# Kernel tuning notes

Measured on AMD Instinct MI355X. Metric: run time of the kernel, lower is better.

The kernel has to match this reference:

```python
import jax, jax.numpy as jnp
import numpy as np

N_NODES = 100_000
N_EDGES = 1_600_000
N_GRAPHS = 512
D_NODE = 128
H = 128
L_EXTRA = 2  # model_layer - 1


def _bn(x, g, b, eps=1e-5):
    # BatchNorm1d, training-mode math (biased batch variance), eval dropout = identity
    mu = jnp.mean(x, axis=0)
    var = jnp.var(x, axis=0)
    return g * (x - mu) * jax.lax.rsqrt(var + eps) + b


def _gin_conv(x, src, dst, W1, b1, bng, bnb, W2, b2):
    # GINConv (eps=0): mlp(x + sum_{j->i} x_j); mlp = Lin -> BN -> ReLU -> Lin
    agg = jax.ops.segment_sum(x[src], dst, num_segments=x.shape[0])
    h = x + agg
    h = jax.nn.relu(_bn(h @ W1 + b1, bng, bnb))
    return h @ W2 + b2


def setup_inputs():
    key = jax.random.key(0)
    ks = jax.random.split(key, 24)
    s = 0.05
    d = {}
    d["x"] = jax.random.normal(ks[0], (N_NODES, D_NODE), dtype=jnp.float32)
    d["edge_index"] = jax.random.randint(ks[1], (2, N_EDGES), 0, N_NODES, dtype=jnp.int32)
    d["batch"] = jnp.sort(jax.random.randint(ks[2], (N_NODES,), 0, N_GRAPHS, dtype=jnp.int32))
    d["vn_emb"] = jax.random.normal(ks[3], (1, H)) * s
    # conv1 MLP: Linear(D_NODE, 2H) -> BN -> ReLU -> Linear(2H, H)
    d["c1_W1"] = jax.random.normal(ks[4], (D_NODE, 2 * H)) * s
    d["c1_b1"] = jnp.zeros((2 * H,))
    d["c1_bng"] = jnp.ones((2 * H,))
    d["c1_bnb"] = jnp.zeros((2 * H,))
    d["c1_W2"] = jax.random.normal(ks[5], (2 * H, H)) * s
    d["c1_b2"] = jnp.zeros((H,))
    d["bn1_g"] = jnp.ones((H,))
    d["bn1_b"] = jnp.zeros((H,))
    # stacked extra GIN layers (model_layer - 1)
    d["cW1"] = jax.random.normal(ks[6], (L_EXTRA, H, 2 * H)) * s
    d["cb1"] = jnp.zeros((L_EXTRA, 2 * H))
    d["cbng"] = jnp.ones((L_EXTRA, 2 * H))
    d["cbnb"] = jnp.zeros((L_EXTRA, 2 * H))
    d["cW2"] = jax.random.normal(ks[7], (L_EXTRA, 2 * H, H)) * s
    d["cb2"] = jnp.zeros((L_EXTRA, H))
    d["bns_g"] = jnp.ones((L_EXTRA, H))
    d["bns_b"] = jnp.zeros((L_EXTRA, H))
    # virtual node MLP: Lin(H,2H)->BN->ReLU->Lin(2H,H)->BN->ReLU->Dropout
    d["vW1"] = jax.random.normal(ks[8], (H, 2 * H)) * s
    d["vb1"] = jnp.zeros((2 * H,))
    d["vbn1_g"] = jnp.ones((2 * H,))
    d["vbn1_b"] = jnp.zeros((2 * H,))
    d["vW2"] = jax.random.normal(ks[9], (2 * H, H)) * s
    d["vb2"] = jnp.zeros((H,))
    d["vbn2_g"] = jnp.ones((H,))
    d["vbn2_b"] = jnp.zeros((H,))
    return d


def reference(x, edge_index, batch, vn_emb, c1_W1, c1_b1, c1_bng, c1_bnb, c1_W2, c1_b2,
              bn1_g, bn1_b, cW1, cb1, cbng, cbnb, cW2, cb2, bns_g, bns_b,
              vW1, vb1, vbn1_g, vbn1_b, vW2, vb2, vbn2_g, vbn2_b):
    src, dst = edge_index[0], edge_index[1]
    # virtual node feature per graph: Embedding(1, H) indexed with zeros
    vfeat = jnp.broadcast_to(vn_emb[0], (N_GRAPHS, H))
    # layer 1: dropout is identity in eval mode
    post = jax.nn.relu(_bn(_gin_conv(x, src, dst, c1_W1, c1_b1, c1_bng, c1_bnb, c1_W2, c1_b2), bn1_g, bn1_b))
    for i in range(L_EXTRA):
        post = post + vfeat[batch]                       # virtual-node broadcast
        post = _bn(_gin_conv(post, src, dst, cW1[i], cb1[i], cbng[i], cbnb[i], cW2[i], cb2[i]), bns_g[i], bns_b[i])
        if i < L_EXTRA - 1:
            post = jax.nn.relu(post)
            pooled = jax.ops.segment_sum(post, batch, num_segments=N_GRAPHS)  # GlobalAddPool
            z = pooled + vfeat
            z = jax.nn.relu(_bn(z @ vW1 + vb1, vbn1_g, vbn1_b))
            vfeat = jax.nn.relu(_bn(z @ vW2 + vb2, vbn2_g, vbn2_b))
    # readout: global mean pool over nodes per graph
    counts = jax.ops.segment_sum(jnp.ones((x.shape[0],), post.dtype), batch, num_segments=N_GRAPHS)
    out = jax.ops.segment_sum(post, batch, num_segments=N_GRAPHS) / jnp.maximum(counts, 1.0)[:, None]
    return out
```

## Files before the change

kernel.cpp:

```cpp
#include <hip/hip_runtime.h>

#define NN 100000
#define NE 1600000
#define NG 512
#define DH 128
#define DH2 256
#define SCB 98
#define NSTRIPE 32

typedef __attribute__((ext_vector_type(8))) _Float16 h8;
typedef __attribute__((ext_vector_type(2))) _Float16 h2;
typedef __attribute__((ext_vector_type(4))) float f4;

static inline size_t align256(size_t x) { return (x + 255) & ~size_t(255); }

__global__ __launch_bounds__(256) void countslot_k(const int* __restrict__ ei,
                                                   int* __restrict__ cursor,
                                                   int* __restrict__ slot) {
    int i = blockIdx.x * blockDim.x + threadIdx.x;
    int e = i * 4;
    if (e >= NE) return;
    int4 d = *(const int4*)(ei + NE + e);
    int s0 = atomicAdd(&cursor[d.x], 1);
    int s1 = atomicAdd(&cursor[d.y], 1);
    int s2 = atomicAdd(&cursor[d.z], 1);
    int s3 = atomicAdd(&cursor[d.w], 1);
    int4 r; r.x = s0; r.y = s1; r.z = s2; r.w = s3;
    *(int4*)(slot + e) = r;
}

__global__ __launch_bounds__(256) void place_k(const int* __restrict__ ei,
                                               const int* __restrict__ rowptr,
                                               const int* __restrict__ slot,
                                               int* __restrict__ esrc) {
    int i = blockIdx.x * blockDim.x + threadIdx.x;
    int e = i * 4;
    if (e >= NE) return;
    int4 d = *(const int4*)(ei + NE + e);
    int4 sl = *(const int4*)(slot + e);
    int4 sr = *(const int4*)(ei + e);
    int r0 = rowptr[d.x];
    int r1 = rowptr[d.y];
    int r2 = rowptr[d.z];
    int r3 = rowptr[d.w];
    esrc[r0 + sl.x] = sr.x;
    esrc[r1 + sl.y] = sr.y;
    esrc[r2 + sl.z] = sr.z;
    esrc[r3 + sl.w] = sr.w;
}

__global__ __launch_bounds__(256) void scan1_k(const int* __restrict__ deg,
                                               int* __restrict__ part) {
    int i0 = blockIdx.x * 1024 + threadIdx.x * 4;
    int s = 0;
    if (i0 < NN) {
        int4 v = *(const int4*)(deg + i0);
        s = v.x + v.y + v.z + v.w;
    }
#pragma unroll
    for (int o = 1; o < 64; o <<= 1) s += __shfl_xor(s, o);
    __shared__ int ws[4];
    if ((threadIdx.x & 63) == 0) ws[threadIdx.x >> 6] = s;
    __syncthreads();
    if (threadIdx.x == 0) part[blockIdx.x] = ws[0] + ws[1] + ws[2] + ws[3];
}

__global__ void scan2_k(int* __restrict__ part, int* __restrict__ rowptr,
                        const int* __restrict__ batch, int* __restrict__ gcnt) {
    int t = threadIdx.x;
    __shared__ int wtot[2];
    int v = 0, s = 0;
    if (t < 128) {
        v = (t < SCB) ? part[t] : 0;
        s = v;
#pragma unroll
        for (int o = 1; o < 64; o <<= 1) {
            int u = __shfl_up(s, o);
            if ((t & 63) >= o) s += u;
        }
        if ((t & 63) == 63) wtot[t >> 6] = s;
    }
    __syncthreads();
    if (t < 128) {
        if (t >= 64) s += wtot[0];
        if (t < SCB) part[t] = s - v;
        if (t == SCB - 1) rowptr[NN] = s;
    }
    for (int g = t; g < NG; g += 256) {
        int lo = 0, hi = NN;
        while (lo < hi) { int m = (lo + hi) >> 1; if (batch[m] < g) lo = m + 1; else hi = m; }
        int b0 = lo;
        lo = 0; hi = NN;
        int g1 = g + 1;
        while (lo < hi) { int m = (lo + hi) >> 1; if (batch[m] < g1) lo = m + 1; else hi = m; }
        gcnt[g] = lo - b0;
    }
}

__global__ __launch_bounds__(256) void scan3_k(const int* __restrict__ deg,
                                               const int* __restrict__ part,
                                               int* __restrict__ rowptr) {
    int t = threadIdx.x;
    int i0 = blockIdx.x * 1024 + t * 4;
    int4 v = {0, 0, 0, 0};
    if (i0 < NN) v = *(const int4*)(deg + i0);
    int s = v.x + v.y + v.z + v.w;
    __shared__ int sc[256];
    sc[t] = s;
    __syncthreads();
    for (int o = 1; o < 256; o <<= 1) {
        int add = (t >= o) ? sc[t - o] : 0;
        __syncthreads();
        sc[t] += add;
        __syncthreads();
    }
    int excl = (t ? sc[t - 1] : 0) + part[blockIdx.x];
    if (i0 < NN) {
        int4 r;
        r.x = excl;
        r.y = excl + v.x;
        r.z = excl + v.x + v.y;
        r.w = excl + v.x + v.y + v.z;
        *(int4*)(rowptr + i0) = r;
    }
}

__global__ void castx_k(const float* __restrict__ x, _Float16* __restrict__ xh,
                        const float* __restrict__ emb, _Float16* __restrict__ vfeat) {
    int i = blockIdx.x * blockDim.x + threadIdx.x;
    if (i < NG * 16) {
        const float* e = emb + (i & 15) * 8;
        h8 v = {(_Float16)e[0], (_Float16)e[1], (_Float16)e[2], (_Float16)e[3],
                (_Float16)e[4], (_Float16)e[5], (_Float16)e[6], (_Float16)e[7]};
        ((h8*)vfeat)[i] = v;
    }
    if (i >= NN * 16) return;
    const float4* s = (const float4*)x + i * 2;
    float4 p = s[0], q = s[1];
    h8 h = {(_Float16)p.x, (_Float16)p.y, (_Float16)p.z, (_Float16)p.w,
            (_Float16)q.x, (_Float16)q.y, (_Float16)q.z, (_Float16)q.w};
    ((h8*)xh)[i] = h;
}

__global__ void zin_k(const float* __restrict__ pooled, const _Float16* __restrict__ vf,
                      _Float16* __restrict__ zb) {
    int i = blockIdx.x * blockDim.x + threadIdx.x;
    if (i < NG * DH) zb[i] = (_Float16)(pooled[i] + (float)vf[i]);
}

__global__ void addvn_k(_Float16* __restrict__ x, const _Float16* __restrict__ vfeat,
                        const int* __restrict__ batch) {
    int i = blockIdx.x * blockDim.x + threadIdx.x;
    if (i >= NN * 16) return;
    int row = i >> 4;
    int bg = batch[row];
    h8 u = ((h8*)x)[i];
    h8 v = ((const h8*)vfeat)[bg * 16 + (i & 15)];
    h8 o;
#pragma unroll
    for (int e = 0; e < 8; e++) o[e] = (_Float16)((float)u[e] + (float)v[e]);
    ((h8*)x)[i] = o;
}

__global__ void finalout_k(const float* __restrict__ pooled2, const int* __restrict__ gcnt,
                           float* __restrict__ outp) {
    int i = blockIdx.x * blockDim.x + threadIdx.x;
    if (i >= NG * DH) return;
    float cnt = (float)gcnt[i >> 7];
    outp[i] = pooled2[i] / fmaxf(cnt, 1.0f);
}

struct WPack {
    const float* w[8];
    _Float16* wt[8];
    int K[8];
    int N[8];
};
__global__ void wtrans_k(WPack p) {
    int id = blockIdx.z;
    const float* W = p.w[id];
    _Float16* Wt = p.wt[id];
    int K = p.K[id], N = p.N[id];
    int n0 = blockIdx.x * 32, k0 = blockIdx.y * 32;
    if (n0 >= N || k0 >= K) return;
    __shared__ float t[32][33];
    int tx = threadIdx.x & 31, ty = threadIdx.x >> 5;
    for (int i = 0; i < 32; i += 8)
        t[ty + i][tx] = W[(size_t)(k0 + ty + i) * N + n0 + tx];
    __syncthreads();
    for (int i = 0; i < 32; i += 8)
        Wt[(size_t)(n0 + ty + i) * K + k0 + tx] = (_Float16)t[tx][ty + i];
}

__global__ __launch_bounds__(256) void agg_k(const _Float16* __restrict__ xin,
                                             const int* __restrict__ rowptr,
                                             const int* __restrict__ esrc,
                                             _Float16* __restrict__ out) {
    int wave = threadIdx.x >> 6, lane = threadIdx.x & 63;
    int node = blockIdx.x * 4 + wave;
    if (node >= NN) return;
    const h2* xr = (const h2*)xin;
    h2 self = xr[(size_t)node * 64 + lane];
    float a0 = (float)self.x, a1 = (float)self.y;
    int beg = rowptr[node], end = rowptr[node + 1];
    int j = beg;
    for (; j + 7 < end; j += 8) {
        int s0 = esrc[j],     s1 = esrc[j + 1], s2 = esrc[j + 2], s3 = esrc[j + 3];
        int s4 = esrc[j + 4], s5 = esrc[j + 5], s6 = esrc[j + 6], s7 = esrc[j + 7];
        h2 u0 = xr[(size_t)s0 * 64 + lane];
        h2 u1 = xr[(size_t)s1 * 64 + lane];
        h2 u2 = xr[(size_t)s2 * 64 + lane];
        h2 u3 = xr[(size_t)s3 * 64 + lane];
        h2 u4 = xr[(size_t)s4 * 64 + lane];
        h2 u5 = xr[(size_t)s5 * 64 + lane];
        h2 u6 = xr[(size_t)s6 * 64 + lane];
        h2 u7 = xr[(size_t)s7 * 64 + lane];
        a0 += ((float)u0.x + (float)u1.x) + ((float)u2.x + (float)u3.x)
            + ((float)u4.x + (float)u5.x) + ((float)u6.x + (float)u7.x);
        a1 += ((float)u0.y + (float)u1.y) + ((float)u2.y + (float)u3.y)
            + ((float)u4.y + (float)u5.y) + ((float)u6.y + (float)u7.y);
    }
    for (; j < end; j++) {
        h2 u = xr[(size_t)esrc[j] * 64 + lane];
        a0 += (float)u.x; a1 += (float)u.y;
    }
    h2 o; o.x = (_Float16)a0; o.y = (_Float16)a1;
    ((h2*)out)[(size_t)node * 64 + lane] = o;
}

__global__ __launch_bounds__(256, 3) void gemmS_k(
        const _Float16* __restrict__ A, const _Float16* __restrict__ Wt,
        const float* __restrict__ bias,
        float* __restrict__ csum, float* __restrict__ csq, int M) {
    constexpr int K = 128;
    constexpr int LDA = K + 8;
    __shared__ __align__(16) _Float16 As[64 * LDA];
    __shared__ __align__(16) _Float16 Ws[128 * LDA];
    const int tid = threadIdx.x;
    const int lane = tid & 63;
    const int wave = tid >> 6;
    const int wr = wave >> 1;
    const int wc = wave & 1;
    const int lm = lane & 15, lq = lane >> 4;
    const int mB = blockIdx.x * 64;

    const int sr = tid >> 4;
    const int sc = (tid & 15) * 8;
#pragma unroll
    for (int rr = 0; rr < 64; rr += 16) {
        int gr = mB + rr + sr; if (gr >= M) gr = M - 1;
        *(h8*)&As[(rr + sr) * LDA + sc] = *(const h8*)&A[(size_t)gr * K + sc];
    }
#pragma unroll
    for (int rr = 0; rr < 128; rr += 16)
        *(h8*)&Ws[(rr + sr) * LDA + sc] = *(const h8*)&Wt[(size_t)(rr + sr) * K + sc];
    __syncthreads();

    f4 acc[2][8];
#pragma unroll
    for (int i = 0; i < 2; i++)
#pragma unroll
        for (int jj = 0; jj < 8; jj++) acc[i][jj] = (f4){0.f, 0.f, 0.f, 0.f};
#pragma unroll
    for (int ct = 0; ct < 2; ct++) {
        if (ct) {
            __syncthreads();
#pragma unroll
            for (int rr = 0; rr < 128; rr += 16)
                *(h8*)&Ws[(rr + sr) * LDA + sc] =
                    *(const h8*)&Wt[(size_t)(128 + rr + sr) * K + sc];
            __syncthreads();
        }
#pragma unroll
        for (int ks = 0; ks < 4; ks++) {
            h8 af[2], bf[4];
#pragma unroll
            for (int i = 0; i < 2; i++)
                af[i] = *(const h8*)&As[(wr * 32 + i * 16 + lm) * LDA + ks * 32 + lq * 8];
#pragma unroll
            for (int j = 0; j < 4; j++)
                bf[j] = *(const h8*)&Ws[(wc * 64 + j * 16 + lm) * LDA + ks * 32 + lq * 8];
#pragma unroll
            for (int i = 0; i < 2; i++)
#pragma unroll
                for (int j = 0; j < 4; j++)
                    acc[i][ct * 4 + j] =
                        __builtin_amdgcn_mfma_f32_16x16x32_f16(af[i], bf[j], acc[i][ct * 4 + j], 0, 0, 0);
        }
    }

    float bv[8];
#pragma unroll
    for (int jj = 0; jj < 8; jj++) bv[jj] = bias[(jj >> 2) * 128 + wc * 64 + (jj & 3) * 16 + lm];
    float ls[8] = {0, 0, 0, 0, 0, 0, 0, 0}, lsq[8] = {0, 0, 0, 0, 0, 0, 0, 0};
#pragma unroll
    for (int i = 0; i < 2; i++) {
        int row = wr * 32 + i * 16 + lq * 4;
#pragma unroll
        for (int jj = 0; jj < 8; jj++) {
#pragma unroll
            for (int r = 0; r < 4; r++) {
                if (mB + row + r < M) {
                    float v = acc[i][jj][r] + bv[jj];
                    ls[jj] += v; lsq[jj] += v * v;
                }
            }
        }
    }
    const int stripe = blockIdx.x & (NSTRIPE - 1);
#pragma unroll
    for (int jj = 0; jj < 8; jj++) {
        float s = ls[jj], q = lsq[jj];
        s += __shfl_xor(s, 16); s += __shfl_xor(s, 32);
        q += __shfl_xor(q, 16); q += __shfl_xor(q, 32);
        if (lq == 0) {
            int col = (jj >> 2) * 128 + wc * 64 + (jj & 3) * 16 + lm;
            atomicAdd(&csum[stripe * 256 + col], s);
            atomicAdd(&csq[stripe * 256 + col], q);
        }
    }
}

__global__ __launch_bounds__(256, 2) void gemmF_k(
        const _Float16* __restrict__ A,
        const _Float16* __restrict__ Wt1,
        const _Float16* __restrict__ Wt2,
        const float* __restrict__ b1v,
        const float* __restrict__ b2v,
        _Float16* __restrict__ C,
        float* __restrict__ csum, float* __restrict__ csq, int M,
        const float* __restrict__ csumIn, const float* __restrict__ csqIn,
        const float* __restrict__ g, const float* __restrict__ b) {
    constexpr int LDA = 136, LDH = 264;
    __shared__ __align__(16) _Float16 Hx[64 * LDH];
    __shared__ __align__(16) _Float16 Ws[128 * LDA];
    __shared__ float s_sc[256], s_sh[256];
    const int tid = threadIdx.x;
    const int lane = tid & 63;
    const int wave = tid >> 6;
    const int wr = wave >> 1;
    const int wc = wave & 1;
    const int lm = lane & 15, lq = lane >> 4;
    const int mB = blockIdx.x * 64;

    {
        float s = 0.f, q = 0.f;
        for (int st = 0; st < NSTRIPE; st++) {
            s += csumIn[st * 256 + tid];
            q += csqIn[st * 256 + tid];
        }
        float invM = 1.0f / (float)M;
        float mean = s * invM;
        float var = q * invM - mean * mean;
        float scv = g[tid] * rsqrtf(var + 1e-5f);
        s_sc[tid] = scv;
        s_sh[tid] = b[tid] - mean * scv;
    }

    const int sr = tid >> 4;
    const int sc = (tid & 15) * 8;
#pragma unroll
    for (int rr = 0; rr < 64; rr += 16) {
        int gr = mB + rr + sr; if (gr >= M) gr = M - 1;
        *(h8*)&Hx[(rr + sr) * LDA + sc] = *(const h8*)&A[(size_t)gr * 128 + sc];
    }
#pragma unroll
    for (int rr = 0; rr < 128; rr += 16)
        *(h8*)&Ws[(rr + sr) * LDA + sc] = *(const h8*)&Wt1[(size_t)(rr + sr) * 128 + sc];
    __syncthreads();

    f4 acc[2][8];
#pragma unroll
    for (int i = 0; i < 2; i++)
#pragma unroll
        for (int jj = 0; jj < 8; jj++) acc[i][jj] = (f4){0.f, 0.f, 0.f, 0.f};
#pragma unroll
    for (int ct = 0; ct < 2; ct++) {
        if (ct) {
            __syncthreads();
#pragma unroll
            for (int rr = 0; rr < 128; rr += 16)
                *(h8*)&Ws[(rr + sr) * LDA + sc] =
                    *(const h8*)&Wt1[(size_t)(128 + rr + sr) * 128 + sc];
            __syncthreads();
        }
#pragma unroll
        for (int ks = 0; ks < 4; ks++) {
            h8 af[2], bf[4];
#pragma unroll
            for (int i = 0; i < 2; i++)
                af[i] = *(const h8*)&Hx[(wr * 32 + i * 16 + lm) * LDA + ks * 32 + lq * 8];
#pragma unroll
            for (int j = 0; j < 4; j++)
                bf[j] = *(const h8*)&Ws[(wc * 64 + j * 16 + lm) * LDA + ks * 32 + lq * 8];
#pragma unroll
            for (int i = 0; i < 2; i++)
#pragma unroll
                for (int j = 0; j < 4; j++)
                    acc[i][ct * 4 + j] =
                        __builtin_amdgcn_mfma_f32_16x16x32_f16(af[i], bf[j], acc[i][ct * 4 + j], 0, 0, 0);
        }
    }
    __syncthreads();

    {
        float bv1[8];
#pragma unroll
        for (int jj = 0; jj < 8; jj++)
            bv1[jj] = b1v[(jj >> 2) * 128 + wc * 64 + (jj & 3) * 16 + lm];
#pragma unroll
        for (int i = 0; i < 2; i++) {
            int row = wr * 32 + i * 16 + lq * 4;
#pragma unroll
            for (int jj = 0; jj < 8; jj++) {
                int col = (jj >> 2) * 128 + wc * 64 + (jj & 3) * 16 + lm;
                float scv = s_sc[col], shv = s_sh[col];
#pragma unroll
                for (int r = 0; r < 4; r++) {
                    float v = acc[i][jj][r] + bv1[jj];
                    v = fmaxf(v * scv + shv, 0.f);
                    Hx[(row + r) * LDH + col] = (_Float16)v;
                }
            }
        }
    }
#pragma unroll
    for (int rr = 0; rr < 128; rr += 16)
        *(h8*)&Ws[(rr + sr) * LDA + sc] = *(const h8*)&Wt2[(size_t)(rr + sr) * 256 + sc];
    __syncthreads();

    f4 acc2[2][4];
#pragma unroll
    for (int i = 0; i < 2; i++)
#pragma unroll
        for (int j = 0; j < 4; j++) acc2[i][j] = (f4){0.f, 0.f, 0.f, 0.f};
#pragma unroll
    for (int kc = 0; kc < 2; kc++) {
        if (kc) {
            __syncthreads();
#pragma unroll
            for (int rr = 0; rr < 128; rr += 16)
                *(h8*)&Ws[(rr + sr) * LDA + sc] =
                    *(const h8*)&Wt2[(size_t)(rr + sr) * 256 + 128 + sc];
            __syncthreads();
        }
#pragma unroll
        for (int ks = 0; ks < 4; ks++) {
            h8 af[2], bf[4];
#pragma unroll
            for (int i = 0; i < 2; i++)
                af[i] = *(const h8*)&Hx[(wr * 32 + i * 16 + lm) * LDH + kc * 128 + ks * 32 + lq * 8];
#pragma unroll
            for (int j = 0; j < 4; j++)
                bf[j] = *(const h8*)&Ws[(wc * 64 + j * 16 + lm) * LDA + ks * 32 + lq * 8];
#pragma unroll
            for (int i = 0; i < 2; i++)
#pragma unroll
                for (int j = 0; j < 4; j++)
                    acc2[i][j] = __builtin_amdgcn_mfma_f32_16x16x32_f16(af[i], bf[j], acc2[i][j], 0, 0, 0);
        }
    }

    const int n0 = wc * 64;
    float bv2[4];
#pragma unroll
    for (int j = 0; j < 4; j++) bv2[j] = b2v[n0 + j * 16 + lm];
    float ls[4] = {0, 0, 0, 0}, lsq[4] = {0, 0, 0, 0};
    __syncthreads();
    _Float16* Cs = Hx;
#pragma unroll
    for (int i = 0; i < 2; i++) {
        int row = wr * 32 + i * 16 + lq * 4;
        bool rv[4];
#pragma unroll
        for (int r = 0; r < 4; r++) rv[r] = (mB + row + r) < M;
#pragma unroll
        for (int j = 0; j < 4; j++) {
#pragma unroll
            for (int r = 0; r < 4; r++) {
                float v = acc2[i][j][r] + bv2[j];
                Cs[(row + r) * LDA + wc * 64 + j * 16 + lm] = (_Float16)v;
                if (rv[r]) { ls[j] += v; lsq[j] += v * v; }
            }
        }
    }
    const int stripe = blockIdx.x & (NSTRIPE - 1);
#pragma unroll
    for (int j = 0; j < 4; j++) {
        float s = ls[j], q = lsq[j];
        s += __shfl_xor(s, 16); s += __shfl_xor(s, 32);
        q += __shfl_xor(q, 16); q += __shfl_xor(q, 32);
        if (lq == 0) {
            atomicAdd(&csum[stripe * 128 + n0 + j * 16 + lm], s);
            atomicAdd(&csq[stripe * 128 + n0 + j * 16 + lm], q);
        }
    }
    __syncthreads();
    const int trow = tid >> 4;
    const int tcol = (tid & 15) * 8;
#pragma unroll
    for (int p = 0; p < 4; p++) {
        int row = p * 16 + trow;
        int grow = mB + row;
        if (grow < M) {
            h8 v = *(const h8*)&Cs[row * LDA + tcol];
            *(h8*)&C[(size_t)grow * 128 + tcol] = v;
        }
    }
}

__global__ void bnrelu_k(const _Float16* __restrict__ in, _Float16* __restrict__ out,
                         const float* __restrict__ csum, const float* __restrict__ csq,
                         const float* __restrict__ g, const float* __restrict__ b,
                         const _Float16* __restrict__ vfeat, const int* __restrict__ batch,
                         int M) {
    constexpr int PER = 16;
    __shared__ float s_sc[128], s_sh[128];
    if (threadIdx.x < 128) {
        int col = threadIdx.x;
        float s = 0.f, q = 0.f;
        for (int st = 0; st < NSTRIPE; st++) {
            s += csum[st * 128 + col];
            q += csq[st * 128 + col];
        }
        float invM = 1.0f / (float)M;
        float mean = s * invM;
        float var = q * invM - mean * mean;
        float scv = g[col] * rsqrtf(var + 1e-5f);
        s_sc[col] = scv;
        s_sh[col] = b[col] - mean * scv;
    }
    __syncthreads();
    int tid = blockIdx.x * blockDim.x + threadIdx.x;
    int c8 = tid % PER;
    int c0 = c8 * 8;
    float sc[8], sh[8];
#pragma unroll
    for (int e = 0; e < 8; e++) { sc[e] = s_sc[c0 + e]; sh[e] = s_sh[c0 + e]; }
    int total = M * PER;
    int stride = gridDim.x * blockDim.x;
    for (int i = tid; i < total; i += stride) {
        int row = i / PER;
        h8 u = ((const h8*)in)[i];
        h8 w;
        bool vn = (vfeat != nullptr);
        if (vn) w = ((const h8*)vfeat)[batch[row] * PER + c8];
        h8 o;
#pragma unroll
        for (int e = 0; e < 8; e++) {
            float vv = fmaxf((float)u[e] * sc[e] + sh[e], 0.f);
            if (vn) vv += (float)w[e];
            o[e] = (_Float16)vv;
        }
        ((h8*)out)[i] = o;
    }
}

__global__ __launch_bounds__(256) void bnpool_k(
        const _Float16* __restrict__ in, _Float16* __restrict__ out,
        const float* __restrict__ csum, const float* __restrict__ csq,
        const float* __restrict__ g, const float* __restrict__ b,
        const int* __restrict__ batch, float* __restrict__ pooled,
        int M, int relu) {
    __shared__ float s_sc[128], s_sh[128];
    if (threadIdx.x < 128) {
        int col = threadIdx.x;
        float s = 0.f, q = 0.f;
        for (int st = 0; st < NSTRIPE; st++) {
            s += csum[st * 128 + col];
            q += csq[st * 128 + col];
        }
        float invM = 1.0f / (float)M;
        float mean = s * invM;
        float var = q * invM - mean * mean;
        float scv = g[col] * rsqrtf(var + 1e-5f);
        s_sc[col] = scv;
        s_sh[col] = b[col] - mean * scv;
    }
    __syncthreads();
    int t = threadIdx.x;
    int c0 = (t & 63) * 2;
    int r0 = blockIdx.x * 128 + (t >> 6) * 32;
    float sc0 = s_sc[c0], h0 = s_sh[c0];
    float sc1 = s_sc[c0 + 1], h1 = s_sh[c0 + 1];
    int rend = r0 + 32; if (rend > M) rend = M;
    float a0 = 0.f, a1 = 0.f; int cur = -1;
    int r = r0;
    for (; r + 1 < rend; r += 2) {
        h2 ua = ((const h2*)in)[(size_t)r * 64 + (c0 >> 1)];
        h2 ub = ((const h2*)in)[(size_t)(r + 1) * 64 + (c0 >> 1)];
        int bga = batch[r], bgb = batch[r + 1];
        float va0 = (float)ua.x * sc0 + h0, va1 = (float)ua.y * sc1 + h1;
        float vb0 = (float)ub.x * sc0 + h0, vb1 = (float)ub.y * sc1 + h1;
        if (relu) {
            va0 = fmaxf(va0, 0.f); va1 = fmaxf(va1, 0.f);
            vb0 = fmaxf(vb0, 0.f); vb1 = fmaxf(vb1, 0.f);
        }
        if (out) {
            h2 oa; oa.x = (_Float16)va0; oa.y = (_Float16)va1;
            h2 ob; ob.x = (_Float16)vb0; ob.y = (_Float16)vb1;
            ((h2*)out)[(size_t)r * 64 + (c0 >> 1)] = oa;
            ((h2*)out)[(size_t)(r + 1) * 64 + (c0 >> 1)] = ob;
        }
        if (bga != cur) {
            if (cur >= 0) {
                atomicAdd(&pooled[(size_t)cur * DH + c0], a0);
                atomicAdd(&pooled[(size_t)cur * DH + c0 + 1], a1);
            }
            cur = bga; a0 = 0.f; a1 = 0.f;
        }
        a0 += va0; a1 += va1;
        if (bgb != cur) {
            atomicAdd(&pooled[(size_t)cur * DH + c0], a0);
            atomicAdd(&pooled[(size_t)cur * DH + c0 + 1], a1);
            cur = bgb; a0 = 0.f; a1 = 0.f;
        }
        a0 += vb0; a1 += vb1;
    }
    for (; r < rend; r++) {
        h2 u = ((const h2*)in)[(size_t)r * 64 + (c0 >> 1)];
        float v0 = (float)u.x * sc0 + h0;
        float v1 = (float)u.y * sc1 + h1;
        if (relu) { v0 = fmaxf(v0, 0.f); v1 = fmaxf(v1, 0.f); }
        if (out) { h2 o; o.x = (_Float16)v0; o.y = (_Float16)v1; ((h2*)out)[(size_t)r * 64 + (c0 >> 1)] = o; }
        int bg = batch[r];
        if (bg != cur) {
            if (cur >= 0) {
                atomicAdd(&pooled[(size_t)cur * DH + c0], a0);
                atomicAdd(&pooled[(size_t)cur * DH + c0 + 1], a1);
            }
            cur = bg; a0 = 0.f; a1 = 0.f;
        }
        a0 += v0; a1 += v1;
    }
    if (cur >= 0) {
        atomicAdd(&pooled[(size_t)cur * DH + c0], a0);
        atomicAdd(&pooled[(size_t)cur * DH + c0 + 1], a1);
    }
}

extern "C" void kernel_launch(void* const* d_in, const int* in_sizes, int n_in,
                              void* d_out, int out_size, void* d_ws, size_t ws_size,
                              hipStream_t stream) {
    const float* x      = (const float*)d_in[0];
    const int*   ei     = (const int*)d_in[1];
    const int*   batch  = (const int*)d_in[2];
    const float* vn_emb = (const float*)d_in[3];
    const float* c1_W1  = (const float*)d_in[4];
    const float* c1_b1  = (const float*)d_in[5];
    const float* c1_bng = (const float*)d_in[6];
    const float* c1_bnb = (const float*)d_in[7];
    const float* c1_W2  = (const float*)d_in[8];
    const float* c1_b2  = (const float*)d_in[9];
    const float* bn1_g  = (const float*)d_in[10];
    const float* bn1_b  = (const float*)d_in[11];
    const float* cW1    = (const float*)d_in[12];
    const float* cb1    = (const float*)d_in[13];
    const float* cbng   = (const float*)d_in[14];
    const float* cbnb   = (const float*)d_in[15];
    const float* cW2    = (const float*)d_in[16];
    const float* cb2    = (const float*)d_in[17];
    const float* bns_g  = (const float*)d_in[18];
    const float* bns_b  = (const float*)d_in[19];
    const float* vW1    = (const float*)d_in[20];
    const float* vb1    = (const float*)d_in[21];
    const float* vbn1_g = (const float*)d_in[22];
    const float* vbn1_b = (const float*)d_in[23];
    const float* vW2    = (const float*)d_in[24];
    const float* vb2    = (const float*)d_in[25];
    const float* vbn2_g = (const float*)d_in[26];
    const float* vbn2_b = (const float*)d_in[27];
    float* outp = (float*)d_out;
    (void)in_sizes; (void)n_in; (void)out_size; (void)ws_size;

    char* w = (char*)d_ws;
    size_t off = 0;
    auto carve = [&](size_t bytes) -> void* {
        void* p = w + off; off = align256(off + bytes); return p;
    };
    int*   cursor  = (int*)carve((size_t)NN * 4);
    float* pooled  = (float*)carve((size_t)NG * DH * 4);
    float* pooled2 = (float*)carve((size_t)NG * DH * 4);
    float *sA[3], *qA[3], *sB[3], *qB[3], *sV1, *qV1, *sV2, *qV2;
    for (int i = 0; i < 3; i++) {
        sA[i] = (float*)carve((size_t)NSTRIPE * 256 * 4);
        qA[i] = (float*)carve((size_t)NSTRIPE * 256 * 4);
    }
    for (int i = 0; i < 3; i++) {
        sB[i] = (float*)carve((size_t)NSTRIPE * 128 * 4);
        qB[i] = (float*)carve((size_t)NSTRIPE * 128 * 4);
    }
    sV1 = (float*)carve((size_t)NSTRIPE * 256 * 4);
    qV1 = (float*)carve((size_t)NSTRIPE * 256 * 4);
    sV2 = (float*)carve((size_t)NSTRIPE * 128 * 4);
    qV2 = (float*)carve((size_t)NSTRIPE * 128 * 4);
    size_t zbytes = off;
    int*   gcnt    = (int*)carve((size_t)NG * 4);
    int*   rowptr  = (int*)carve((size_t)(NN + 1) * 4);
    int*   slot    = (int*)carve((size_t)NE * 4);
    int*   esrc    = (int*)carve((size_t)NE * 4);
    int*   part    = (int*)carve((size_t)SCB * 4);
    _Float16* vfeat = (_Float16*)carve((size_t)NG * DH * 2);
    _Float16* zin   = (_Float16*)carve((size_t)NG * DH * 2);
    _Float16* vraw  = (_Float16*)carve((size_t)NG * DH * 2);
    _Float16* xh    = (_Float16*)carve((size_t)NN * DH * 2);
    _Float16* hb    = (_Float16*)carve((size_t)NN * DH * 2);
    _Float16* abuf  = (_Float16*)carve((size_t)NN * DH * 2);
    _Float16* Wt[8];
    for (int i = 0; i < 8; i++) Wt[i] = (_Float16*)carve((size_t)DH * DH2 * 2);

    WPack wp;
    wp.w[0] = c1_W1;            wp.K[0] = 128; wp.N[0] = 256;
    wp.w[1] = c1_W2;            wp.K[1] = 256; wp.N[1] = 128;
    wp.w[2] = cW1;              wp.K[2] = 128; wp.N[2] = 256;
    wp.w[3] = cW2;              wp.K[3] = 256; wp.N[3] = 128;
    wp.w[4] = cW1 + 128 * 256;  wp.K[4] = 128; wp.N[4] = 256;
    wp.w[5] = cW2 + 256 * 128;  wp.K[5] = 256; wp.N[5] = 128;
    wp.w[6] = vW1;              wp.K[6] = 128; wp.N[6] = 256;
    wp.w[7] = vW2;              wp.K[7] = 256; wp.N[7] = 128;
    for (int i = 0; i < 8; i++) wp.wt[i] = Wt[i];

    const int GB64 = (NN + 63) / 64;
    const int GB   = (NN + 127) / 128;
    const int GV64 = (NG + 63) / 64;
    const int EB4  = (NE / 4 + 255) / 256;

    hipMemsetAsync(d_ws, 0, zbytes, stream);
    countslot_k<<<EB4, 256, 0, stream>>>(ei, cursor, slot);
    scan1_k<<<SCB, 256, 0, stream>>>(cursor, part);
    scan2_k<<<1, 256, 0, stream>>>(part, rowptr, batch, gcnt);
    scan3_k<<<SCB, 256, 0, stream>>>(cursor, part, rowptr);
    place_k<<<EB4, 256, 0, stream>>>(ei, rowptr, slot, esrc);
    wtrans_k<<<dim3(8, 8, 8), 256, 0, stream>>>(wp);
    castx_k<<<(NN * 16 + 255) / 256, 256, 0, stream>>>(x, xh, vn_emb, vfeat);

    agg_k<<<NN / 4, 256, 0, stream>>>(xh, rowptr, esrc, hb);
    gemmS_k<<<GB64, 256, 0, stream>>>(hb, Wt[0], c1_b1, sA[0], qA[0], NN);
    gemmF_k<<<GB64, 256, 0, stream>>>(hb, Wt[0], Wt[1], c1_b1, c1_b2, abuf,
                                      sB[0], qB[0], NN, sA[0], qA[0], c1_bng, c1_bnb);
    bnrelu_k<<<2048, 256, 0, stream>>>(abuf, abuf, sB[0], qB[0], bn1_g, bn1_b,
                                       vfeat, batch, NN);

    agg_k<<<NN / 4, 256, 0, stream>>>(abuf, rowptr, esrc, hb);
    gemmS_k<<<GB64, 256, 0, stream>>>(hb, Wt[2], cb1, sA[1], qA[1], NN);
    gemmF_k<<<GB64, 256, 0, stream>>>(hb, Wt[2], Wt[3], cb1, cb2, abuf,
                                      sB[1], qB[1], NN, sA[1], qA[1], cbng, cbnb);
    bnpool_k<<<GB, 256, 0, stream>>>(abuf, abuf, sB[1], qB[1], bns_g, bns_b,
                                     batch, pooled, NN, 1);

    zin_k<<<(NG * DH + 255) / 256, 256, 0, stream>>>(pooled, vfeat, zin);
    gemmS_k<<<GV64, 256, 0, stream>>>(zin, Wt[6], vb1, sV1, qV1, NG);
    gemmF_k<<<GV64, 256, 0, stream>>>(zin, Wt[6], Wt[7], vb1, vb2, vraw,
                                      sV2, qV2, NG, sV1, qV1, vbn1_g, vbn1_b);
    bnrelu_k<<<32, 256, 0, stream>>>(vraw, vfeat, sV2, qV2, vbn2_g, vbn2_b,
                                     nullptr, nullptr, NG);

    addvn_k<<<(NN * 16 + 255) / 256, 256, 0, stream>>>(abuf, vfeat, batch);
    agg_k<<<NN / 4, 256, 0, stream>>>(abuf, rowptr, esrc, hb);
    gemmS_k<<<GB64, 256, 0, stream>>>(hb, Wt[4], cb1 + 256, sA[2], qA[2], NN);
    gemmF_k<<<GB64, 256, 0, stream>>>(hb, Wt[4], Wt[5], cb1 + 256, cb2 + 128, abuf,
                                      sB[2], qB[2], NN, sA[2], qA[2], cbng + 256, cbnb + 256);
    bnpool_k<<<GB, 256, 0, stream>>>(abuf, nullptr, sB[2], qB[2],
                                     bns_g + 128, bns_b + 128, batch, pooled2, NN, 0);

    finalout_k<<<(NG * DH + 255) / 256, 256, 0, stream>>>(pooled2, gcnt, outp);
}
```

Before: 713.9 us.

## Split degree-count atomics into four sub-counters and fuse cast into CSR count kernel

The edge-count kernel now spreads its atomics over four separate counter arrays, one per lane of each int4 edge group. This is meant to cut contention on popular destination nodes. The scan kernels sum the four arrays and write per-sub-counter base offsets, which place_k uses to scatter sources. The x-to-fp16 cast is folded into the same launch as extra blocks, removing one kernel launch. The cost is a larger zeroed cursor region and an extra 1.6MB rowbase array written and read during the scans.

```diff
diff --git a/kernel.cpp b/kernel.cpp
--- a/kernel.cpp
+++ b/kernel.cpp
@@ -7,6 +7,8 @@
 #define DH2 256
 #define SCB 98
 #define NSTRIPE 32
+#define EB4 1563
+#define CB 6250
 
 typedef __attribute__((ext_vector_type(8))) _Float16 h8;
 typedef __attribute__((ext_vector_type(2))) _Float16 h2;
@@ -14,23 +16,41 @@
 
 static inline size_t align256(size_t x) { return (x + 255) & ~size_t(255); }
 
-__global__ __launch_bounds__(256) void countslot_k(const int* __restrict__ ei,
-                                                   int* __restrict__ cursor,
-                                                   int* __restrict__ slot) {
-    int i = blockIdx.x * blockDim.x + threadIdx.x;
-    int e = i * 4;
-    if (e >= NE) return;
-    int4 d = *(const int4*)(ei + NE + e);
-    int s0 = atomicAdd(&cursor[d.x], 1);
-    int s1 = atomicAdd(&cursor[d.y], 1);
-    int s2 = atomicAdd(&cursor[d.z], 1);
-    int s3 = atomicAdd(&cursor[d.w], 1);
-    int4 r; r.x = s0; r.y = s1; r.z = s2; r.w = s3;
-    *(int4*)(slot + e) = r;
+__global__ __launch_bounds__(256) void csrcast_k(
+        const int* __restrict__ ei, int* __restrict__ cursor, int* __restrict__ slot,
+        const float* __restrict__ x, _Float16* __restrict__ xh,
+        const float* __restrict__ emb, _Float16* __restrict__ vfeat) {
+    int b = blockIdx.x;
+    if (b < EB4) {
+        int i = b * 256 + threadIdx.x;
+        int e = i * 4;
+        if (e >= NE) return;
+        int4 d = *(const int4*)(ei + NE + e);
+        int s0 = atomicAdd(&cursor[0 * NN + d.x], 1);
+        int s1 = atomicAdd(&cursor[1 * NN + d.y], 1);
+        int s2 = atomicAdd(&cursor[2 * NN + d.z], 1);
+        int s3 = atomicAdd(&cursor[3 * NN + d.w], 1);
+        int4 r; r.x = s0; r.y = s1; r.z = s2; r.w = s3;
+        *(int4*)(slot + e) = r;
+    } else {
+        int i = (b - EB4) * 256 + threadIdx.x;
+        if (i < NG * 16) {
+            const float* e = emb + (i & 15) * 8;
+            h8 v = {(_Float16)e[0], (_Float16)e[1], (_Float16)e[2], (_Float16)e[3],
+                    (_Float16)e[4], (_Float16)e[5], (_Float16)e[6], (_Float16)e[7]};
+            ((h8*)vfeat)[i] = v;
+        }
+        if (i >= NN * 16) return;
+        const float4* s = (const float4*)x + i * 2;
+        float4 p = s[0], q = s[1];
+        h8 h = {(_Float16)p.x, (_Float16)p.y, (_Float16)p.z, (_Float16)p.w,
+                (_Float16)q.x, (_Float16)q.y, (_Float16)q.z, (_Float16)q.w};
+        ((h8*)xh)[i] = h;
+    }
 }
 
 __global__ __launch_bounds__(256) void place_k(const int* __restrict__ ei,
-                                               const int* __restrict__ rowptr,
+                                               const int* __restrict__ rowbase,
                                                const int* __restrict__ slot,
                                                int* __restrict__ esrc) {
     int i = blockIdx.x * blockDim.x + threadIdx.x;
@@ -39,23 +59,27 @@
     int4 d = *(const int4*)(ei + NE + e);
     int4 sl = *(const int4*)(slot + e);
     int4 sr = *(const int4*)(ei + e);
-    int r0 = rowptr[d.x];
-    int r1 = rowptr[d.y];
-    int r2 = rowptr[d.z];
-    int r3 = rowptr[d.w];
+    int r0 = rowbase[0 * NN + d.x];
+    int r1 = rowbase[1 * NN + d.y];
+    int r2 = rowbase[2 * NN + d.z];
+    int r3 = rowbase[3 * NN + d.w];
     esrc[r0 + sl.x] = sr.x;
     esrc[r1 + sl.y] = sr.y;
     esrc[r2 + sl.z] = sr.z;
     esrc[r3 + sl.w] = sr.w;
 }
 
-__global__ __launch_bounds__(256) void scan1_k(const int* __restrict__ deg,
+__global__ __launch_bounds__(256) void scan1_k(const int* __restrict__ cur,
                                                int* __restrict__ part) {
     int i0 = blockIdx.x * 1024 + threadIdx.x * 4;
     int s = 0;
     if (i0 < NN) {
-        int4 v = *(const int4*)(deg + i0);
-        s = v.x + v.y + v.z + v.w;
+        int4 a = *(const int4*)(cur + i0);
+        int4 b = *(const int4*)(cur + NN + i0);
+        int4 c = *(const int4*)(cur + 2 * NN + i0);
+        int4 d = *(const int4*)(cur + 3 * NN + i0);
+        s = (a.x + a.y + a.z + a.w) + (b.x + b.y + b.z + b.w)
+          + (c.x + c.y + c.z + c.w) + (d.x + d.y + d.z + d.w);
     }
 #pragma unroll
     for (int o = 1; o < 64; o <<= 1) s += __shfl_xor(s, o);
@@ -97,14 +121,25 @@
     }
 }
 
-__global__ __launch_bounds__(256) void scan3_k(const int* __restrict__ deg,
+__global__ __launch_bounds__(256) void scan3_k(const int* __restrict__ cur,
                                                const int* __restrict__ part,
-                                               int* __restrict__ rowptr) {
+                                               int* __restrict__ rowptr,
+                                               int* __restrict__ rowbase) {
     int t = threadIdx.x;
     int i0 = blockIdx.x * 1024 + t * 4;
-    int4 v = {0, 0, 0, 0};
-    if (i0 < NN) v = *(const int4*)(deg + i0);
-    int s = v.x + v.y + v.z + v.w;
+    int4 c0 = {0,0,0,0}, c1 = {0,0,0,0}, c2 = {0,0,0,0}, c3 = {0,0,0,0};
+    if (i0 < NN) {
+        c0 = *(const int4*)(cur + i0);
+        c1 = *(const int4*)(cur + NN + i0);
+        c2 = *(const int4*)(cur + 2 * NN + i0);
+        c3 = *(const int4*)(cur + 3 * NN + i0);
+    }
+    int4 tot;
+    tot.x = c0.x + c1.x + c2.x + c3.x;
+    tot.y = c0.y + c1.y + c2.y + c3.y;
+    tot.z = c0.z + c1.z + c2.z + c3.z;
+    tot.w = c0.w + c1.w + c2.w + c3.w;
+    int s = tot.x + tot.y + tot.z + tot.w;
     __shared__ int sc[256];
     sc[t] = s;
     __syncthreads();
@@ -118,28 +153,18 @@
     if (i0 < NN) {
         int4 r;
         r.x = excl;
-        r.y = excl + v.x;
-        r.z = excl + v.x + v.y;
-        r.w = excl + v.x + v.y + v.z;
+        r.y = excl + tot.x;
+        r.z = r.y + tot.y;
+        r.w = r.z + tot.z;
         *(int4*)(rowptr + i0) = r;
-    }
-}
-
-__global__ void castx_k(const float* __restrict__ x, _Float16* __restrict__ xh,
-                        const float* __restrict__ emb, _Float16* __restrict__ vfeat) {
-    int i = blockIdx.x * blockDim.x + threadIdx.x;
-    if (i < NG * 16) {
-        const float* e = emb + (i & 15) * 8;
-        h8 v = {(_Float16)e[0], (_Float16)e[1], (_Float16)e[2], (_Float16)e[3],
-                (_Float16)e[4], (_Float16)e[5], (_Float16)e[6], (_Float16)e[7]};
-        ((h8*)vfeat)[i] = v;
-    }
-    if (i >= NN * 16) return;
-    const float4* s = (const float4*)x + i * 2;
-    float4 p = s[0], q = s[1];
-    h8 h = {(_Float16)p.x, (_Float16)p.y, (_Float16)p.z, (_Float16)p.w,
-            (_Float16)q.x, (_Float16)q.y, (_Float16)q.z, (_Float16)q.w};
-    ((h8*)xh)[i] = h;
+        *(int4*)(rowbase + i0) = r;
+        int4 b1v; b1v.x = r.x + c0.x; b1v.y = r.y + c0.y; b1v.z = r.z + c0.z; b1v.w = r.w + c0.w;
+        *(int4*)(rowbase + NN + i0) = b1v;
+        int4 b2v; b2v.x = b1v.x + c1.x; b2v.y = b1v.y + c1.y; b2v.z = b1v.z + c1.z; b2v.w = b1v.w + c1.w;
+        *(int4*)(rowbase + 2 * NN + i0) = b2v;
+        int4 b3v; b3v.x = b2v.x + c2.x; b3v.y = b2v.y + c2.y; b3v.z = b2v.z + c2.z; b3v.w = b2v.w + c2.w;
+        *(int4*)(rowbase + 3 * NN + i0) = b3v;
+    }
 }
 
 __global__ void zin_k(const float* __restrict__ pooled, const _Float16* __restrict__ vf,
@@ -678,7 +703,7 @@
     auto carve = [&](size_t bytes) -> void* {
         void* p = w + off; off = align256(off + bytes); return p;
     };
-    int*   cursor  = (int*)carve((size_t)NN * 4);
+    int*   cursor  = (int*)carve((size_t)4 * NN * 4);
     float* pooled  = (float*)carve((size_t)NG * DH * 4);
     float* pooled2 = (float*)carve((size_t)NG * DH * 4);
     float *sA[3], *qA[3], *sB[3], *qB[3], *sV1, *qV1, *sV2, *qV2;
@@ -697,6 +722,7 @@
     size_t zbytes = off;
     int*   gcnt    = (int*)carve((size_t)NG * 4);
     int*   rowptr  = (int*)carve((size_t)(NN + 1) * 4);
+    int*   rowbase = (int*)carve((size_t)4 * NN * 4);
     int*   slot    = (int*)carve((size_t)NE * 4);
     int*   esrc    = (int*)carve((size_t)NE * 4);
     int*   part    = (int*)carve((size_t)SCB * 4);
@@ -723,16 +749,14 @@
     const int GB64 = (NN + 63) / 64;
     const int GB   = (NN + 127) / 128;
     const int GV64 = (NG + 63) / 64;
-    const int EB4  = (NE / 4 + 255) / 256;
 
     hipMemsetAsync(d_ws, 0, zbytes, stream);
-    countslot_k<<<EB4, 256, 0, stream>>>(ei, cursor, slot);
+    csrcast_k<<<EB4 + CB, 256, 0, stream>>>(ei, cursor, slot, x, xh, vn_emb, vfeat);
     scan1_k<<<SCB, 256, 0, stream>>>(cursor, part);
     scan2_k<<<1, 256, 0, stream>>>(part, rowptr, batch, gcnt);
-    scan3_k<<<SCB, 256, 0, stream>>>(cursor, part, rowptr);
-    place_k<<<EB4, 256, 0, stream>>>(ei, rowptr, slot, esrc);
+    scan3_k<<<SCB, 256, 0, stream>>>(cursor, part, rowptr, rowbase);
+    place_k<<<EB4, 256, 0, stream>>>(ei, rowbase, slot, esrc);
     wtrans_k<<<dim3(8, 8, 8), 256, 0, stream>>>(wp);
-    castx_k<<<(NN * 16 + 255) / 256, 256, 0, stream>>>(x, xh, vn_emb, vfeat);
 
     agg_k<<<NN / 4, 256, 0, stream>>>(xh, rowptr, esrc, hb);
     gemmS_k<<<GB64, 256, 0, stream>>>(hb, Wt[0], c1_b1, sA[0], qA[0], NN);
```

New measurement: 705.0 us. About the same (-1.2%).
